# Optimization experiments

Hardware: AMD Instinct MI355X
Metric: run time of the kernel (lower is better)

## Reference

```python
import jax, jax.numpy as jnp
import numpy as np

MXFP_BLOCK = 32
FP32_MIN_NORMAL = 2.0 ** (-126)
# fp8_e4m3 element format params (bit_width=8)
EXP_BITS = 4
MBITS = 8            # mantissa bits incl. sign, used as 2**(MBITS-2) fixed-point scale
EMAX = 8
MAX_NORM = 448.0     # 2**8 * 1.75
SCALE_EMAX = 127.0   # 2**(MXFP_SCALE_BITS-1) - 1
MIN_PEXP = -6.0      # -2**(EXP_BITS-1) + 2


def _round_away(x):
    return jnp.sign(x) * jnp.floor(jnp.abs(x) + 0.5)


def mxfp_quant_lastdim(x):
    """Block-wise MXFP fp8_e4m3 fake quant along the last dim (block=32, no padding needed)."""
    shape = x.shape
    xb = x.reshape(shape[:-1] + (shape[-1] // MXFP_BLOCK, MXFP_BLOCK))
    shared = jnp.max(jnp.abs(xb), axis=-1, keepdims=True)
    zero_mask = (shared == 0).astype(xb.dtype)
    shared_exp = jnp.floor(jnp.log2(shared + FP32_MIN_NORMAL * zero_mask)) - EMAX
    shared_exp = jnp.where(shared_exp > SCALE_EMAX, jnp.nan, shared_exp)
    shared_exp = jnp.maximum(shared_exp, -SCALE_EMAX)
    scale = jnp.exp2(shared_exp)
    v = xb / scale
    # per-element private exponent, fixed-point mantissa rounding
    pexp = jnp.floor(jnp.log2(jnp.abs(v) + (v == 0).astype(v.dtype)))
    pexp = jnp.maximum(pexp, MIN_PEXP)
    pscale = jnp.exp2(pexp)
    m = 2.0 ** (MBITS - 2)  # 64
    q = _round_away(v / pscale * m) * pscale / m
    q = jnp.clip(q, -MAX_NORM, MAX_NORM)
    return (q * scale).reshape(shape)


def setup_inputs() -> dict:
    key = jax.random.key(0)
    k1, k2, k3 = jax.random.split(key, 3)
    B, S, DIN, DOUT = 8, 8192, 1024, 1024
    x = jax.random.normal(k1, (B, S, DIN), dtype=jnp.float32)
    weight = jax.random.normal(k2, (DOUT, DIN), dtype=jnp.float32) * 0.02
    bias = jax.random.normal(k3, (DOUT,), dtype=jnp.float32) * 0.02
    return {"x": x, "weight": weight, "bias": bias}


def reference(x, weight, bias):
    xq = mxfp_quant_lastdim(x)          # per-token blocks along features
    wq = mxfp_quant_lastdim(weight)     # per-output-channel blocks along in_features
    return jnp.einsum('bsd,od->bso', xq, wq) + bias
```

## Files before the change

kernel.cpp:

```cpp
#include <hip/hip_runtime.h>
#include <cstdint>
#include <cstddef>

#define MM 65536
#define NN 1024
#define KK 1024

typedef __bf16 bf16x8 __attribute__((ext_vector_type(8)));
typedef float f32x4 __attribute__((ext_vector_type(4)));

typedef const __attribute__((address_space(1))) unsigned int* gas_t;
typedef __attribute__((address_space(3))) unsigned int* las_t;

__device__ __forceinline__ void gll16(const void* g, void* l) {
  __builtin_amdgcn_global_load_lds((gas_t)g, (las_t)l, 16, 0, 0);
}

__device__ __forceinline__ float exp2i(int e) {
  return __int_as_float((e + 127) << 23);
}

__global__ __launch_bounds__(256) void mxfp_quant(const float* __restrict__ in,
                                                  unsigned short* __restrict__ out) {
  size_t i = (size_t)blockIdx.x * 256 + threadIdx.x;
  float4 v = ((const float4*)in)[i];
  float a = fmaxf(fmaxf(fabsf(v.x), fabsf(v.y)), fmaxf(fabsf(v.z), fabsf(v.w)));
  a = fmaxf(a, __shfl_xor(a, 1));
  a = fmaxf(a, __shfl_xor(a, 2));
  a = fmaxf(a, __shfl_xor(a, 4));
  int ebits = (int)((__float_as_uint(a) >> 23) & 0xff);
  int se = (ebits > 0 ? ebits : 1) - 127 - 8;
  se = se < -126 ? -126 : se;
  float sinv = exp2i(-se);
  float sc = exp2i(se);

  float e[4] = {v.x, v.y, v.z, v.w};
  unsigned short o[4];
#pragma unroll
  for (int c = 0; c < 4; ++c) {
    float vv = e[c] * sinv;
    int pe = (int)((__float_as_uint(vv) >> 23) & 0xff) - 127;
    pe = pe < -6 ? -6 : pe;
    float r = floorf(fabsf(vv) * exp2i(6 - pe) + 0.5f);
    float q = copysignf(r * exp2i(pe - 6), vv);
    q = fminf(fmaxf(q, -448.f), 448.f);
    float res = q * sc;
    o[c] = (unsigned short)(__float_as_uint(res) >> 16);
  }
  ushort4 ov = {o[0], o[1], o[2], o[3]};
  ((ushort4*)out)[i] = ov;
}

__global__ __launch_bounds__(256, 3) void gemm_bt(const unsigned short* __restrict__ A,
                                                  const unsigned short* __restrict__ B,
                                                  const float* __restrict__ bias,
                                                  float* __restrict__ C) {
  __shared__ unsigned short As[128 * 32];
  __shared__ unsigned short Bs[128 * 32];
  int t = threadIdx.x;
  int bx = blockIdx.x & 7;
  int by = blockIdx.x >> 3;
  int m0 = by << 7, n0 = bx << 7;

  int lr = t >> 2;
  int lc = (t & 3) << 4;
  const char* Ag = (const char*)A + (size_t)(m0 + lr) * (KK * 2) + lc;
  const char* Bg = (const char*)B + (size_t)(n0 + lr) * (KK * 2) + lc;
  char* AsB = (char*)As + t * 16;
  char* BsB = (char*)Bs + t * 16;

  int lane = t & 63, w = t >> 6;
  int wm = (w & 1) << 6, wn = (w >> 1) << 6;
  int quad = lane >> 4, r16 = lane & 15;

  f32x4 acc[4][4] = {};

  for (int kt = 0; kt < KK; kt += 32) {
    __syncthreads();
    size_t go = (size_t)kt * 2;
    gll16(Ag + go, AsB);
    gll16(Ag + go + (size_t)64 * KK * 2, AsB + 4096);
    gll16(Bg + go, BsB);
    gll16(Bg + go + (size_t)64 * KK * 2, BsB + 4096);
    __syncthreads();

    bf16x8 af[4], bf[4];
#pragma unroll
    for (int i = 0; i < 4; ++i)
      af[i] = *(const bf16x8*)&As[(wm + i * 16 + r16) * 32 + quad * 8];
#pragma unroll
    for (int j = 0; j < 4; ++j)
      bf[j] = *(const bf16x8*)&Bs[(wn + j * 16 + r16) * 32 + quad * 8];
#pragma unroll
    for (int i = 0; i < 4; ++i)
#pragma unroll
      for (int j = 0; j < 4; ++j)
        acc[i][j] = __builtin_amdgcn_mfma_f32_16x16x32_bf16(af[i], bf[j], acc[i][j], 0, 0, 0);
  }

  float bcol[4];
#pragma unroll
  for (int j = 0; j < 4; ++j) bcol[j] = bias[n0 + wn + j * 16 + r16];
#pragma unroll
  for (int i = 0; i < 4; ++i) {
    int rbase = m0 + wm + i * 16 + quad * 4;
#pragma unroll
    for (int j = 0; j < 4; ++j) {
      int col = n0 + wn + j * 16 + r16;
      float* Cp = C + (size_t)rbase * NN + col;
#pragma unroll
      for (int reg = 0; reg < 4; ++reg)
        Cp[(size_t)reg * NN] = acc[i][j][reg] + bcol[j];
    }
  }
}

extern "C" void kernel_launch(void* const* d_in, const int* in_sizes, int n_in,
                              void* d_out, int out_size, void* d_ws, size_t ws_size,
                              hipStream_t stream) {
  const float* x = (const float*)d_in[0];
  const float* wgt = (const float*)d_in[1];
  const float* bias = (const float*)d_in[2];
  float* out = (float*)d_out;

  unsigned short* xq = (unsigned short*)d_ws;
  unsigned short* wq = xq + (size_t)MM * KK;

  mxfp_quant<<<(MM * (size_t)KK) / 1024, 256, 0, stream>>>(x, xq);
  mxfp_quant<<<(NN * (size_t)KK) / 1024, 256, 0, stream>>>(wgt, wq);
  gemm_bt<<<(MM / 128) * (NN / 128), 256, 0, stream>>>(xq, wq, bias, out);
}
```

Baseline: 614.0 us.

## Rewrite GEMM with 256x256 tiles, double-buffered swizzled LDS and interleaved prefetch

Replaces the 128x128, 256-thread, single-buffered GEMM with a 256x256 tile computed by 512 threads over K-steps of 64. Next-tile global-to-LDS loads are issued in chunks between MFMA phases, with vmcnt waits, barriers and s_setprio. The LDS layout gains an XOR swizzle to avoid bank conflicts, and the block index is remapped for L2 locality. The goal is to hide memory latency behind MFMA work and raise arithmetic intensity. The cost is 128KB of LDS per block, many barriers, and heavy register pressure from 32 accumulators.

Measured after the change: 594.1 us. 1.03x faster.

```diff
diff --git a/kernel.cpp b/kernel.cpp
--- a/kernel.cpp
+++ b/kernel.cpp
@@ -5,6 +5,7 @@
 #define MM 65536
 #define NN 1024
 #define KK 1024
+#define NT 16
 
 typedef __bf16 bf16x8 __attribute__((ext_vector_type(8)));
 typedef float f32x4 __attribute__((ext_vector_type(4)));
@@ -18,6 +19,10 @@
 
 __device__ __forceinline__ float exp2i(int e) {
   return __int_as_float((e + 127) << 23);
+}
+
+__device__ __forceinline__ f32x4 mfma(bf16x8 a, bf16x8 b, f32x4 c) {
+  return __builtin_amdgcn_mfma_f32_16x16x32_bf16(a, b, c, 0, 0, 0);
 }
 
 __global__ __launch_bounds__(256) void mxfp_quant(const float* __restrict__ in,
@@ -51,68 +56,136 @@
   ((ushort4*)out)[i] = ov;
 }
 
-__global__ __launch_bounds__(256, 3) void gemm_bt(const unsigned short* __restrict__ A,
+__global__ __launch_bounds__(512, 2) void gemm_bt(const unsigned short* __restrict__ A,
                                                   const unsigned short* __restrict__ B,
                                                   const float* __restrict__ bias,
                                                   float* __restrict__ C) {
-  __shared__ unsigned short As[128 * 32];
-  __shared__ unsigned short Bs[128 * 32];
-  int t = threadIdx.x;
-  int bx = blockIdx.x & 7;
-  int by = blockIdx.x >> 3;
-  int m0 = by << 7, n0 = bx << 7;
-
-  int lr = t >> 2;
-  int lc = (t & 3) << 4;
-  const char* Ag = (const char*)A + (size_t)(m0 + lr) * (KK * 2) + lc;
-  const char* Bg = (const char*)B + (size_t)(n0 + lr) * (KK * 2) + lc;
-  char* AsB = (char*)As + t * 16;
-  char* BsB = (char*)Bs + t * 16;
-
-  int lane = t & 63, w = t >> 6;
-  int wm = (w & 1) << 6, wn = (w >> 1) << 6;
-  int quad = lane >> 4, r16 = lane & 15;
-
-  f32x4 acc[4][4] = {};
-
-  for (int kt = 0; kt < KK; kt += 32) {
-    __syncthreads();
-    size_t go = (size_t)kt * 2;
-    gll16(Ag + go, AsB);
-    gll16(Ag + go + (size_t)64 * KK * 2, AsB + 4096);
-    gll16(Bg + go, BsB);
-    gll16(Bg + go + (size_t)64 * KK * 2, BsB + 4096);
-    __syncthreads();
-
-    bf16x8 af[4], bf[4];
-#pragma unroll
-    for (int i = 0; i < 4; ++i)
-      af[i] = *(const bf16x8*)&As[(wm + i * 16 + r16) * 32 + quad * 8];
-#pragma unroll
-    for (int j = 0; j < 4; ++j)
-      bf[j] = *(const bf16x8*)&Bs[(wn + j * 16 + r16) * 32 + quad * 8];
-#pragma unroll
-    for (int i = 0; i < 4; ++i)
-#pragma unroll
-      for (int j = 0; j < 4; ++j)
-        acc[i][j] = __builtin_amdgcn_mfma_f32_16x16x32_bf16(af[i], bf[j], acc[i][j], 0, 0, 0);
+  __shared__ unsigned short As[2][256 * 64];
+  __shared__ unsigned short Bs[2][256 * 64];
+  const int t = threadIdx.x;
+  const int wg = ((blockIdx.x & 7) << 7) | (blockIdx.x >> 3);
+  const int m0 = (wg >> 2) << 8;
+  const int n0 = (wg & 3) << 8;
+
+  const int lane = t & 63, w = t >> 6;
+  const int wm = (w >> 2) << 7;
+  const int wn = (w & 3) << 6;
+  const int quad = lane >> 4, r16 = lane & 15;
+
+  const int rt = t >> 3;
+  const int cl = (t & 7) ^ (rt & 7);
+  const unsigned short* Ag = A + (size_t)(m0 + rt) * KK + cl * 8;
+  const unsigned short* Bg = B + (size_t)(n0 + rt) * KK + cl * 8;
+  char* AsW = (char*)As + t * 16;
+  char* BsW = (char*)Bs + t * 16;
+  const char* AsR = (const char*)As + (wm + r16) * 128;
+  const char* BsR = (const char*)Bs + (wn + r16) * 128;
+  const int sw0 = (quad ^ (r16 & 7)) << 4;
+  const int sw1 = ((4 | quad) ^ (r16 & 7)) << 4;
+
+#define STG_A(BUF, H, C_, T_)                                                     \
+  gll16(Ag + (size_t)((H) * 128 + (C_) * 64) * KK + (size_t)(T_) * 64,            \
+        AsW + (BUF) * 32768 + (H) * 16384 + (C_) * 8192)
+#define STG_B(BUF, H, C_, T_)                                                     \
+  gll16(Bg + (size_t)((H) * 128 + (C_) * 64) * KK + (size_t)(T_) * 64,            \
+        BsW + (BUF) * 32768 + (H) * 16384 + (C_) * 8192)
+#define LDA(BUF, MP, SW) (*(const bf16x8*)(AsR + (BUF) * 32768 + (MP) * 2048 + (SW)))
+#define LDB(BUF, NP, SW) (*(const bf16x8*)(BsR + (BUF) * 32768 + (NP) * 2048 + (SW)))
+#define MFMA16(MB)                                              \
+  do {                                                          \
+    acc[(MB) + 0][0] = mfma(a0, b0, acc[(MB) + 0][0]);          \
+    acc[(MB) + 0][1] = mfma(a0, b1, acc[(MB) + 0][1]);          \
+    acc[(MB) + 0][2] = mfma(a0, b2, acc[(MB) + 0][2]);          \
+    acc[(MB) + 0][3] = mfma(a0, b3, acc[(MB) + 0][3]);          \
+    acc[(MB) + 1][0] = mfma(a1, b0, acc[(MB) + 1][0]);          \
+    acc[(MB) + 1][1] = mfma(a1, b1, acc[(MB) + 1][1]);          \
+    acc[(MB) + 1][2] = mfma(a1, b2, acc[(MB) + 1][2]);          \
+    acc[(MB) + 1][3] = mfma(a1, b3, acc[(MB) + 1][3]);          \
+    acc[(MB) + 2][0] = mfma(a2, b0, acc[(MB) + 2][0]);          \
+    acc[(MB) + 2][1] = mfma(a2, b1, acc[(MB) + 2][1]);          \
+    acc[(MB) + 2][2] = mfma(a2, b2, acc[(MB) + 2][2]);          \
+    acc[(MB) + 2][3] = mfma(a2, b3, acc[(MB) + 2][3]);          \
+    acc[(MB) + 3][0] = mfma(a3, b0, acc[(MB) + 3][0]);          \
+    acc[(MB) + 3][1] = mfma(a3, b1, acc[(MB) + 3][1]);          \
+    acc[(MB) + 3][2] = mfma(a3, b2, acc[(MB) + 3][2]);          \
+    acc[(MB) + 3][3] = mfma(a3, b3, acc[(MB) + 3][3]);          \
+  } while (0)
+
+  f32x4 acc[8][4] = {};
+
+  STG_A(0, 0, 0, 0); STG_A(0, 0, 1, 0);
+  STG_A(0, 1, 0, 0); STG_A(0, 1, 1, 0);
+  STG_B(0, 0, 0, 0); STG_B(0, 0, 1, 0);
+  STG_B(0, 1, 0, 0); STG_B(0, 1, 1, 0);
+
+#pragma unroll 2
+  for (int kt = 0; kt < NT; ++kt) {
+    const int bi = kt & 1;
+    const int nx = bi ^ 1;
+    const bool pf = (kt + 1) < NT;
+    bf16x8 a0, a1, a2, a3, b0, b1, b2, b3;
+
+    if (pf) {
+      STG_A(nx, 0, 0, kt + 1); STG_A(nx, 0, 1, kt + 1);
+      asm volatile("s_waitcnt vmcnt(2)" ::: "memory");
+    } else {
+      asm volatile("s_waitcnt vmcnt(0)" ::: "memory");
+    }
+    __builtin_amdgcn_s_barrier();
+    asm volatile("" ::: "memory");
+    a0 = LDA(bi, 0, sw0); a1 = LDA(bi, 1, sw0); a2 = LDA(bi, 2, sw0); a3 = LDA(bi, 3, sw0);
+    b0 = LDB(bi, 0, sw0); b1 = LDB(bi, 1, sw0); b2 = LDB(bi, 2, sw0); b3 = LDB(bi, 3, sw0);
+    __builtin_amdgcn_s_setprio(1);
+    MFMA16(0);
+    __builtin_amdgcn_s_setprio(0);
+    __builtin_amdgcn_s_barrier();
+
+    a0 = LDA(bi, 4, sw0); a1 = LDA(bi, 5, sw0); a2 = LDA(bi, 6, sw0); a3 = LDA(bi, 7, sw0);
+    if (pf) { STG_A(nx, 1, 0, kt + 1); STG_A(nx, 1, 1, kt + 1); }
+    __builtin_amdgcn_s_barrier();
+    __builtin_amdgcn_s_setprio(1);
+    MFMA16(4);
+    __builtin_amdgcn_s_setprio(0);
+    __builtin_amdgcn_s_barrier();
+
+    a0 = LDA(bi, 0, sw1); a1 = LDA(bi, 1, sw1); a2 = LDA(bi, 2, sw1); a3 = LDA(bi, 3, sw1);
+    b0 = LDB(bi, 0, sw1); b1 = LDB(bi, 1, sw1); b2 = LDB(bi, 2, sw1); b3 = LDB(bi, 3, sw1);
+    if (pf) { STG_B(nx, 0, 0, kt + 1); STG_B(nx, 0, 1, kt + 1); }
+    __builtin_amdgcn_s_barrier();
+    __builtin_amdgcn_s_setprio(1);
+    MFMA16(0);
+    __builtin_amdgcn_s_setprio(0);
+    __builtin_amdgcn_s_barrier();
+
+    a0 = LDA(bi, 4, sw1); a1 = LDA(bi, 5, sw1); a2 = LDA(bi, 6, sw1); a3 = LDA(bi, 7, sw1);
+    if (pf) { STG_B(nx, 1, 0, kt + 1); STG_B(nx, 1, 1, kt + 1); }
+    __builtin_amdgcn_s_barrier();
+    __builtin_amdgcn_s_setprio(1);
+    MFMA16(4);
+    __builtin_amdgcn_s_setprio(0);
+    __builtin_amdgcn_s_barrier();
   }
 
   float bcol[4];
 #pragma unroll
   for (int j = 0; j < 4; ++j) bcol[j] = bias[n0 + wn + j * 16 + r16];
 #pragma unroll
-  for (int i = 0; i < 4; ++i) {
-    int rbase = m0 + wm + i * 16 + quad * 4;
+  for (int mp = 0; mp < 8; ++mp) {
+    const int rbase = m0 + wm + mp * 16 + quad * 4;
 #pragma unroll
     for (int j = 0; j < 4; ++j) {
-      int col = n0 + wn + j * 16 + r16;
+      const int col = n0 + wn + j * 16 + r16;
       float* Cp = C + (size_t)rbase * NN + col;
 #pragma unroll
       for (int reg = 0; reg < 4; ++reg)
-        Cp[(size_t)reg * NN] = acc[i][j][reg] + bcol[j];
+        Cp[(size_t)reg * NN] = acc[mp][j][reg] + bcol[j];
     }
   }
+#undef STG_A
+#undef STG_B
+#undef LDA
+#undef LDB
+#undef MFMA16
 }
 
 extern "C" void kernel_launch(void* const* d_in, const int* in_sizes, int n_in,
@@ -128,5 +201,5 @@
 
   mxfp_quant<<<(MM * (size_t)KK) / 1024, 256, 0, stream>>>(x, xq);
   mxfp_quant<<<(NN * (size_t)KK) / 1024, 256, 0, stream>>>(wgt, wq);
-  gemm_bt<<<(MM / 128) * (NN / 128), 256, 0, stream>>>(xq, wq, bias, out);
-}
+  gemm_bt<<<(MM / 256) * (NN / 256), 512, 0, stream>>>(xq, wq, bias, out);
+}
```
